# Performance work log

Measured on AMD Instinct MI355X. Metric: run time of the kernel, lower is better.

## Reference

```python
import jax, jax.numpy as jnp
import numpy as np

NUM_TABLES = 10
EMB_DIM = 3
VOCAB = 1_000_000
N_IDX = 4_000_000
N_BAGS = 100_000


def setup_inputs() -> dict:
    key = jax.random.key(0)
    k_idx, k_off, k_w = jax.random.split(key, 3)
    eb_input = jax.random.randint(k_idx, (N_IDX,), 0, VOCAB, dtype=jnp.int64)
    # EmbeddingBag offsets: sorted, first element must be 0, values in [0, N_IDX)
    eb_offset = jnp.sort(jax.random.randint(k_off, (N_BAGS,), 0, N_IDX, dtype=jnp.int64))
    eb_offset = eb_offset.at[0].set(0)
    # torch.nn.EmbeddingBag default init: N(0, 1)
    W = jax.random.normal(k_w, (NUM_TABLES, VOCAB, EMB_DIM), dtype=jnp.float32)
    return {"eb_input": eb_input, "eb_offset": eb_offset, "W": W}


def _bag_sums(eb_input, eb_offset, W):
    # segment id for each index position: bag b covers [offset[b], offset[b+1])
    n = eb_input.shape[0]
    seg = jnp.searchsorted(eb_offset, jnp.arange(n), side="right") - 1  # [N]
    gathered = W[:, eb_input, :]  # [T, N, D] irregular gather
    # sum-pool per bag for every table
    per_bag = jax.vmap(lambda g: jax.ops.segment_sum(g, seg, num_segments=eb_offset.shape[0]))(gathered)  # [T, B, D]
    return per_bag


def reference(eb_input, eb_offset, W):
    per_bag = _bag_sums(eb_input, eb_offset, W)  # [10, B, 3]
    outs = [per_bag[i] for i in range(NUM_TABLES)]
    outs[5] = jnp.sum(outs[5], axis=1, keepdims=True)  # [B, 1]
    outs[6] = jnp.sum(outs[6], axis=1, keepdims=True)  # [B, 1]
    cat = jnp.concatenate(outs, axis=1)  # [B, 26]
    return jnp.sum(cat, axis=0)  # [26]
```

## Files before the change

### kernel.cpp

```cpp
#include <hip/hip_runtime.h>

#define VOCAB 1000000
#define NUM_TABLES 10
#define OUT_SIZE 26
#define BUCKET_BITS 12
#define BPB 4096
#define NBUCKETS 245
#define CHUNK 4096
#define MAXSRC 1024
#define RBLOCKS_PER_TABLE 128
#define RTHREADS 256


__global__ void __launch_bounds__(256) scatter_kernel(
    const int* __restrict__ idx, int n,
    unsigned short* __restrict__ scat,
    unsigned int* __restrict__ gs32)
{
    __shared__ unsigned int lcount[256];
    __shared__ unsigned int sc[256];
    const int tid = threadIdx.x;
    lcount[tid] = 0u;
    __syncthreads();

    const int4* idx4 = (const int4*)idx;
    const int n4 = n >> 2;
    const int base4 = blockIdx.x * (CHUNK / 4);
    int4 q[4];
    bool val[4];
    unsigned rank[16];
    unsigned bkt[16];
#pragma unroll
    for (int j = 0; j < 4; ++j) {
        int i4 = base4 + j * 256 + tid;
        val[j] = (i4 < n4);
        if (val[j]) q[j] = idx4[i4];
    }
#pragma unroll
    for (int j = 0; j < 4; ++j) {
        if (val[j]) {
            unsigned v[4] = {(unsigned)q[j].x, (unsigned)q[j].y, (unsigned)q[j].z, (unsigned)q[j].w};
#pragma unroll
            for (int e = 0; e < 4; ++e) {
                bkt[j * 4 + e] = v[e] >> BUCKET_BITS;
                rank[j * 4 + e] = atomicAdd(&lcount[bkt[j * 4 + e]], 1u);
            }
        }
    }
    unsigned trank[3], tbkt[3];
    int tcnt = 0;
    if (blockIdx.x == gridDim.x - 1 && tid == 0) {
        for (int i = n4 * 4; i < n; ++i) {
            unsigned u = (unsigned)idx[i];
            tbkt[tcnt] = u >> BUCKET_BITS;
            trank[tcnt] = atomicAdd(&lcount[tbkt[tcnt]], 1u);
            ++tcnt;
        }
    }
    __syncthreads();
    unsigned cnt = (tid < NBUCKETS) ? lcount[tid] : 0u;
    sc[tid] = cnt;
    __syncthreads();
#pragma unroll
    for (int off = 1; off < 256; off <<= 1) {
        unsigned v = sc[tid];
        unsigned a = (tid >= off) ? sc[tid - off] : 0u;
        __syncthreads();
        sc[tid] = v + a;
        __syncthreads();
    }
    unsigned excl = sc[tid] - cnt;
    if (tid < NBUCKETS) gs32[tid * MAXSRC + blockIdx.x] = excl | (cnt << 16);
    lcount[tid] = excl;
    __syncthreads();
    unsigned short* myscat = scat + (size_t)blockIdx.x * CHUNK;
#pragma unroll
    for (int j = 0; j < 4; ++j) {
        if (val[j]) {
            unsigned v[4] = {(unsigned)q[j].x, (unsigned)q[j].y, (unsigned)q[j].z, (unsigned)q[j].w};
#pragma unroll
            for (int e = 0; e < 4; ++e) {
                unsigned k = j * 4 + e;
                myscat[lcount[bkt[k]] + rank[k]] = (unsigned short)(v[e] & (BPB - 1));
            }
        }
    }
    if (blockIdx.x == gridDim.x - 1 && tid == 0) {
        for (int i = 0; i < tcnt; ++i) {
            unsigned u = (unsigned)idx[n4 * 4 + i];
            myscat[lcount[tbkt[i]] + trank[i]] = (unsigned short)(u & (BPB - 1));
        }
    }
}

__device__ inline float wave_reduce(float v) {
#pragma unroll
    for (int o = 32; o > 0; o >>= 1) v += __shfl_down(v, o, 64);
    return v;
}

__global__ void __launch_bounds__(1024) fused_kernel(
    const unsigned short* __restrict__ scat,
    const unsigned int* __restrict__ gs32, int nsrc,
    const float* __restrict__ W,
    float* __restrict__ partials)
{
    __shared__ unsigned int h[BPB];
    const int b = blockIdx.x;
    const int tid = threadIdx.x;
    for (int i = tid; i < BPB; i += 1024) h[i] = 0u;
    __syncthreads();
    if (tid < nsrc) {
        unsigned g32 = gs32[b * MAXSRC + tid];
        unsigned s = g32 & 0xffffu, c = g32 >> 16;
        const unsigned short* p = scat + (size_t)tid * CHUNK + s;
        for (unsigned k = 0; k < c; ++k) atomicAdd(&h[p[k]], 1u);
    }
    __syncthreads();

    float acc[NUM_TABLES][3];
#pragma unroll
    for (int t = 0; t < NUM_TABLES; ++t) { acc[t][0] = 0.f; acc[t][1] = 0.f; acc[t][2] = 0.f; }

    const int ngroups = min(BPB / 4, (VOCAB - b * BPB) / 4);
    const int g = tid;
    if (g < ngroups) {
        uint4 c4 = ((const uint4*)h)[g];
        float c0 = (float)c4.x, c1 = (float)c4.y, c2 = (float)c4.z, c3 = (float)c4.w;
        size_t w4base = (size_t)b * 3072 + 3 * (size_t)g;
#pragma unroll
        for (int t = 0; t < NUM_TABLES; ++t) {
            const float4* W4 = ((const float4*)W) + (size_t)t * 750000 + w4base;
            float4 w0 = W4[0];
            float4 w1 = W4[1];
            float4 w2 = W4[2];
            acc[t][0] += c0 * w0.x + c1 * w0.w + c2 * w1.z + c3 * w2.y;
            acc[t][1] += c0 * w0.y + c1 * w1.x + c2 * w1.w + c3 * w2.z;
            acc[t][2] += c0 * w0.z + c1 * w1.y + c2 * w2.x + c3 * w2.w;
        }
    }
    __syncthreads();
    float* sf = (float*)h;
    const int wave = tid >> 6, lane = tid & 63;
#pragma unroll
    for (int t = 0; t < NUM_TABLES; ++t)
#pragma unroll
        for (int d = 0; d < 3; ++d) {
            float v = wave_reduce(acc[t][d]);
            if (lane == 0) sf[(t * 3 + d) * 16 + wave] = v;
        }
    __syncthreads();
    if (tid < 30) {
        float s = 0.f;
#pragma unroll
        for (int w = 0; w < 16; ++w) s += sf[tid * 16 + w];
        partials[b * 32 + tid] = s;
    }
}

__global__ void __launch_bounds__(256) final_kernel(const float* __restrict__ partials,
                                                    float* __restrict__ out) {
    __shared__ float red[256];
    __shared__ float tot[32];
    const int tid = threadIdx.x;
    const int v = tid & 31, c = tid >> 5;
    float s = 0.f;
    if (v < 30)
        for (int b = c; b < NBUCKETS; b += 8) s += partials[b * 32 + v];
    red[tid] = s;
    __syncthreads();
    if (tid < 32) {
        float t2 = 0.f;
#pragma unroll
        for (int cc = 0; cc < 8; ++cc) t2 += red[cc * 32 + tid];
        tot[tid] = t2;
    }
    __syncthreads();
    if (tid < OUT_SIZE) {
        float r;
        if (tid < 15) r = tot[tid];
        else if (tid == 15) r = tot[15] + tot[16] + tot[17];
        else if (tid == 16) r = tot[18] + tot[19] + tot[20];
        else r = tot[tid + 4];
        out[tid] = r;
    }
}


__global__ void zero_kernel_fb(unsigned int* __restrict__ hist, float* __restrict__ out) {
    int i = blockIdx.x * blockDim.x + threadIdx.x;
    int n4 = VOCAB / 4;
    if (i < n4) ((uint4*)hist)[i] = make_uint4(0u, 0u, 0u, 0u);
    if (i < OUT_SIZE) out[i] = 0.0f;
}

__global__ void hist_kernel_fb(const int* __restrict__ idx, unsigned int* __restrict__ hist, int n) {
    int i = blockIdx.x * blockDim.x + threadIdx.x;
    int i4 = i * 4;
    if (i4 + 3 < n) {
        int4 v = ((const int4*)idx)[i];
        atomicAdd(&hist[v.x], 1u);
        atomicAdd(&hist[v.y], 1u);
        atomicAdd(&hist[v.z], 1u);
        atomicAdd(&hist[v.w], 1u);
    } else {
        for (int j = i4; j < n; ++j) atomicAdd(&hist[idx[j]], 1u);
    }
}

__global__ void __launch_bounds__(RTHREADS) reduce_kernel_fb(const float* __restrict__ W,
                                                             const unsigned int* __restrict__ hist,
                                                             float* __restrict__ out) {
    const int t = blockIdx.x / RBLOCKS_PER_TABLE;
    const int b = blockIdx.x % RBLOCKS_PER_TABLE;
    const float4* __restrict__ W4 = (const float4*)(W + (size_t)t * VOCAB * 3);
    const uint4* __restrict__ h4 = (const uint4*)hist;
    const int ngroups = VOCAB / 4;
    float a0 = 0.f, a1 = 0.f, a2 = 0.f;
    const int stride = RBLOCKS_PER_TABLE * RTHREADS;
    for (int g = b * RTHREADS + (int)threadIdx.x; g < ngroups; g += stride) {
        uint4 c4 = h4[g];
        float4 w0 = W4[3 * g + 0];
        float4 w1 = W4[3 * g + 1];
        float4 w2 = W4[3 * g + 2];
        float c0 = (float)c4.x, c1 = (float)c4.y, c2 = (float)c4.z, c3 = (float)c4.w;
        a0 += c0 * w0.x + c1 * w0.w + c2 * w1.z + c3 * w2.y;
        a1 += c0 * w0.y + c1 * w1.x + c2 * w1.w + c3 * w2.z;
        a2 += c0 * w0.z + c1 * w1.y + c2 * w2.x + c3 * w2.w;
    }
    a0 = wave_reduce(a0);
    a1 = wave_reduce(a1);
    a2 = wave_reduce(a2);
    __shared__ float s[3][4];
    int wave = threadIdx.x >> 6;
    int lane = threadIdx.x & 63;
    if (lane == 0) { s[0][wave] = a0; s[1][wave] = a1; s[2][wave] = a2; }
    __syncthreads();
    if (threadIdx.x == 0) {
        float r0 = s[0][0] + s[0][1] + s[0][2] + s[0][3];
        float r1 = s[1][0] + s[1][1] + s[1][2] + s[1][3];
        float r2 = s[2][0] + s[2][1] + s[2][2] + s[2][3];
        if (t == 5) atomicAdd(&out[15], r0 + r1 + r2);
        else if (t == 6) atomicAdd(&out[16], r0 + r1 + r2);
        else {
            int base = (t < 5) ? t * 3 : 17 + (t - 7) * 3;
            atomicAdd(&out[base + 0], r0);
            atomicAdd(&out[base + 1], r1);
            atomicAdd(&out[base + 2], r2);
        }
    }
}


extern "C" void kernel_launch(void* const* d_in, const int* in_sizes, int n_in,
                              void* d_out, int out_size, void* d_ws, size_t ws_size,
                              hipStream_t stream) {
    const int* eb_input = (const int*)d_in[0];
    const float* W = (const float*)d_in[2];
    float* out = (float*)d_out;
    int n_idx = in_sizes[0];

    const int nsrc = (n_idx + CHUNK - 1) / CHUNK;
    const size_t scat_bytes = (size_t)MAXSRC * CHUNK * 2;
    const size_t gs_off = scat_bytes;
    const size_t gs_bytes = (size_t)NBUCKETS * MAXSRC * 4;
    const size_t part_off = gs_off + gs_bytes;
    const size_t need = part_off + (size_t)NBUCKETS * 32 * 4;

    if (nsrc <= MAXSRC && ws_size >= need) {
        unsigned short* scat = (unsigned short*)d_ws;
        unsigned int* gs32 = (unsigned int*)((char*)d_ws + gs_off);
        float* partials = (float*)((char*)d_ws + part_off);

        scatter_kernel<<<nsrc, 256, 0, stream>>>(eb_input, n_idx, scat, gs32);
        fused_kernel<<<NBUCKETS, 1024, 0, stream>>>(scat, gs32, nsrc, W, partials);
        final_kernel<<<1, 256, 0, stream>>>(partials, out);
    } else {
        unsigned int* hist = (unsigned int*)d_ws;
        int zblocks = (VOCAB / 4 + 255) / 256;
        zero_kernel_fb<<<zblocks, 256, 0, stream>>>(hist, out);
        int hthreads = (n_idx + 3) / 4;
        int hblocks = (hthreads + 255) / 256;
        hist_kernel_fb<<<hblocks, 256, 0, stream>>>(eb_input, hist, n_idx);
        reduce_kernel_fb<<<NUM_TABLES * RBLOCKS_PER_TABLE, RTHREADS, 0, stream>>>(W, hist, out);
    }
}
```

Baseline: 235.1 us.

## Split fused bucket kernel into histogram and wide reduce kernels, stage scatter in LDS

The per-bucket histogram-plus-weight kernel is split in two. A bucket histogram kernel writes a full global histogram, then a separate reduce kernel with many more blocks (10 tables × 256) streams W, writes per-block partials, and a new final kernel sums them. The goal is to spread the 120 MB W read across many more blocks than the 245 used before. The scatter kernel now stages its output in shared memory and writes it out with coalesced 16-byte stores, and the histogram loop is unrolled by four. The cost is an extra kernel launch plus a 4 MB histogram round trip through global memory.

```diff
diff --git a/kernel.cpp b/kernel.cpp
--- a/kernel.cpp
+++ b/kernel.cpp
@@ -8,7 +8,8 @@
 #define NBUCKETS 245
 #define CHUNK 4096
 #define MAXSRC 1024
-#define RBLOCKS_PER_TABLE 128
+#define RBLOCKS_PER_TABLE 256
+#define NRBLK (NUM_TABLES * RBLOCKS_PER_TABLE)
 #define RTHREADS 256
 
 
@@ -19,6 +20,7 @@
 {
     __shared__ unsigned int lcount[256];
     __shared__ unsigned int sc[256];
+    __shared__ unsigned short stage[CHUNK];
     const int tid = threadIdx.x;
     lcount[tid] = 0u;
     __syncthreads();
@@ -73,7 +75,6 @@
     if (tid < NBUCKETS) gs32[tid * MAXSRC + blockIdx.x] = excl | (cnt << 16);
     lcount[tid] = excl;
     __syncthreads();
-    unsigned short* myscat = scat + (size_t)blockIdx.x * CHUNK;
 #pragma unroll
     for (int j = 0; j < 4; ++j) {
         if (val[j]) {
@@ -81,29 +82,27 @@
 #pragma unroll
             for (int e = 0; e < 4; ++e) {
                 unsigned k = j * 4 + e;
-                myscat[lcount[bkt[k]] + rank[k]] = (unsigned short)(v[e] & (BPB - 1));
+                stage[lcount[bkt[k]] + rank[k]] = (unsigned short)(v[e] & (BPB - 1));
             }
         }
     }
     if (blockIdx.x == gridDim.x - 1 && tid == 0) {
         for (int i = 0; i < tcnt; ++i) {
             unsigned u = (unsigned)idx[n4 * 4 + i];
-            myscat[lcount[tbkt[i]] + trank[i]] = (unsigned short)(u & (BPB - 1));
-        }
-    }
-}
-
-__device__ inline float wave_reduce(float v) {
-#pragma unroll
-    for (int o = 32; o > 0; o >>= 1) v += __shfl_down(v, o, 64);
-    return v;
-}
-
-__global__ void __launch_bounds__(1024) fused_kernel(
+            stage[lcount[tbkt[i]] + trank[i]] = (unsigned short)(u & (BPB - 1));
+        }
+    }
+    __syncthreads();
+    uint4* dst = (uint4*)(scat + (size_t)blockIdx.x * CHUNK);
+    const uint4* src = (const uint4*)stage;
+#pragma unroll
+    for (int j = 0; j < 2; ++j) dst[j * 256 + tid] = src[j * 256 + tid];
+}
+
+__global__ void __launch_bounds__(1024) bucket_hist_kernel(
     const unsigned short* __restrict__ scat,
     const unsigned int* __restrict__ gs32, int nsrc,
-    const float* __restrict__ W,
-    float* __restrict__ partials)
+    unsigned int* __restrict__ hist)
 {
     __shared__ unsigned int h[BPB];
     const int b = blockIdx.x;
@@ -114,103 +113,32 @@
         unsigned g32 = gs32[b * MAXSRC + tid];
         unsigned s = g32 & 0xffffu, c = g32 >> 16;
         const unsigned short* p = scat + (size_t)tid * CHUNK + s;
-        for (unsigned k = 0; k < c; ++k) atomicAdd(&h[p[k]], 1u);
-    }
-    __syncthreads();
-
-    float acc[NUM_TABLES][3];
-#pragma unroll
-    for (int t = 0; t < NUM_TABLES; ++t) { acc[t][0] = 0.f; acc[t][1] = 0.f; acc[t][2] = 0.f; }
-
-    const int ngroups = min(BPB / 4, (VOCAB - b * BPB) / 4);
-    const int g = tid;
-    if (g < ngroups) {
-        uint4 c4 = ((const uint4*)h)[g];
-        float c0 = (float)c4.x, c1 = (float)c4.y, c2 = (float)c4.z, c3 = (float)c4.w;
-        size_t w4base = (size_t)b * 3072 + 3 * (size_t)g;
-#pragma unroll
-        for (int t = 0; t < NUM_TABLES; ++t) {
-            const float4* W4 = ((const float4*)W) + (size_t)t * 750000 + w4base;
-            float4 w0 = W4[0];
-            float4 w1 = W4[1];
-            float4 w2 = W4[2];
-            acc[t][0] += c0 * w0.x + c1 * w0.w + c2 * w1.z + c3 * w2.y;
-            acc[t][1] += c0 * w0.y + c1 * w1.x + c2 * w1.w + c3 * w2.z;
-            acc[t][2] += c0 * w0.z + c1 * w1.y + c2 * w2.x + c3 * w2.w;
-        }
-    }
-    __syncthreads();
-    float* sf = (float*)h;
-    const int wave = tid >> 6, lane = tid & 63;
-#pragma unroll
-    for (int t = 0; t < NUM_TABLES; ++t)
-#pragma unroll
-        for (int d = 0; d < 3; ++d) {
-            float v = wave_reduce(acc[t][d]);
-            if (lane == 0) sf[(t * 3 + d) * 16 + wave] = v;
-        }
-    __syncthreads();
-    if (tid < 30) {
-        float s = 0.f;
-#pragma unroll
-        for (int w = 0; w < 16; ++w) s += sf[tid * 16 + w];
-        partials[b * 32 + tid] = s;
-    }
-}
-
-__global__ void __launch_bounds__(256) final_kernel(const float* __restrict__ partials,
-                                                    float* __restrict__ out) {
-    __shared__ float red[256];
-    __shared__ float tot[32];
-    const int tid = threadIdx.x;
-    const int v = tid & 31, c = tid >> 5;
-    float s = 0.f;
-    if (v < 30)
-        for (int b = c; b < NBUCKETS; b += 8) s += partials[b * 32 + v];
-    red[tid] = s;
-    __syncthreads();
-    if (tid < 32) {
-        float t2 = 0.f;
-#pragma unroll
-        for (int cc = 0; cc < 8; ++cc) t2 += red[cc * 32 + tid];
-        tot[tid] = t2;
-    }
-    __syncthreads();
-    if (tid < OUT_SIZE) {
-        float r;
-        if (tid < 15) r = tot[tid];
-        else if (tid == 15) r = tot[15] + tot[16] + tot[17];
-        else if (tid == 16) r = tot[18] + tot[19] + tot[20];
-        else r = tot[tid + 4];
-        out[tid] = r;
-    }
-}
-
-
-__global__ void zero_kernel_fb(unsigned int* __restrict__ hist, float* __restrict__ out) {
-    int i = blockIdx.x * blockDim.x + threadIdx.x;
-    int n4 = VOCAB / 4;
-    if (i < n4) ((uint4*)hist)[i] = make_uint4(0u, 0u, 0u, 0u);
-    if (i < OUT_SIZE) out[i] = 0.0f;
-}
-
-__global__ void hist_kernel_fb(const int* __restrict__ idx, unsigned int* __restrict__ hist, int n) {
-    int i = blockIdx.x * blockDim.x + threadIdx.x;
-    int i4 = i * 4;
-    if (i4 + 3 < n) {
-        int4 v = ((const int4*)idx)[i];
-        atomicAdd(&hist[v.x], 1u);
-        atomicAdd(&hist[v.y], 1u);
-        atomicAdd(&hist[v.z], 1u);
-        atomicAdd(&hist[v.w], 1u);
-    } else {
-        for (int j = i4; j < n; ++j) atomicAdd(&hist[idx[j]], 1u);
-    }
-}
-
-__global__ void __launch_bounds__(RTHREADS) reduce_kernel_fb(const float* __restrict__ W,
-                                                             const unsigned int* __restrict__ hist,
-                                                             float* __restrict__ out) {
+        unsigned k = 0;
+        for (; k + 4 <= c; k += 4) {
+            unsigned short a0 = p[k], a1 = p[k + 1], a2 = p[k + 2], a3 = p[k + 3];
+            atomicAdd(&h[a0], 1u);
+            atomicAdd(&h[a1], 1u);
+            atomicAdd(&h[a2], 1u);
+            atomicAdd(&h[a3], 1u);
+        }
+        for (; k < c; ++k) atomicAdd(&h[p[k]], 1u);
+    }
+    __syncthreads();
+    int nb4 = min(BPB, VOCAB - b * BPB) >> 2;
+    uint4* dst = (uint4*)(hist + (size_t)b * BPB);
+    const uint4* src = (const uint4*)h;
+    if (tid < nb4) dst[tid] = src[tid];
+}
+
+__device__ inline float wave_reduce(float v) {
+#pragma unroll
+    for (int o = 32; o > 0; o >>= 1) v += __shfl_down(v, o, 64);
+    return v;
+}
+
+__global__ void __launch_bounds__(RTHREADS) reduce_kernel(const float* __restrict__ W,
+                                                          const unsigned int* __restrict__ hist,
+                                                          float* __restrict__ partials) {
     const int t = blockIdx.x / RBLOCKS_PER_TABLE;
     const int b = blockIdx.x % RBLOCKS_PER_TABLE;
     const float4* __restrict__ W4 = (const float4*)(W + (size_t)t * VOCAB * 3);
@@ -237,6 +165,90 @@
     if (lane == 0) { s[0][wave] = a0; s[1][wave] = a1; s[2][wave] = a2; }
     __syncthreads();
     if (threadIdx.x == 0) {
+        partials[0 * NRBLK + blockIdx.x] = s[0][0] + s[0][1] + s[0][2] + s[0][3];
+        partials[1 * NRBLK + blockIdx.x] = s[1][0] + s[1][1] + s[1][2] + s[1][3];
+        partials[2 * NRBLK + blockIdx.x] = s[2][0] + s[2][1] + s[2][2] + s[2][3];
+    }
+}
+
+__global__ void __launch_bounds__(1024) final_kernel(const float* __restrict__ partials,
+                                                     float* __restrict__ out) {
+    __shared__ float ts[32];
+    const int tid = threadIdx.x;
+    const int srs = tid >> 5;
+    const int j = tid & 31;
+    float v = 0.f;
+    if (srs < 30) {
+        const int t = srs / 3, d = srs % 3;
+        const float* p = partials + (size_t)d * NRBLK + t * RBLOCKS_PER_TABLE;
+#pragma unroll
+        for (int k = 0; k < RBLOCKS_PER_TABLE / 32; ++k) v += p[k * 32 + j];
+    }
+#pragma unroll
+    for (int off = 16; off > 0; off >>= 1) v += __shfl_down(v, off);
+    if (j == 0 && srs < 30) ts[srs] = v;
+    __syncthreads();
+    if (tid < OUT_SIZE) {
+        float r;
+        if (tid < 15) r = ts[tid];
+        else if (tid == 15) r = ts[15] + ts[16] + ts[17];
+        else if (tid == 16) r = ts[18] + ts[19] + ts[20];
+        else r = ts[tid + 4];
+        out[tid] = r;
+    }
+}
+
+
+__global__ void zero_kernel_fb(unsigned int* __restrict__ hist, float* __restrict__ out) {
+    int i = blockIdx.x * blockDim.x + threadIdx.x;
+    int n4 = VOCAB / 4;
+    if (i < n4) ((uint4*)hist)[i] = make_uint4(0u, 0u, 0u, 0u);
+    if (i < OUT_SIZE) out[i] = 0.0f;
+}
+
+__global__ void hist_kernel_fb(const int* __restrict__ idx, unsigned int* __restrict__ hist, int n) {
+    int i = blockIdx.x * blockDim.x + threadIdx.x;
+    int i4 = i * 4;
+    if (i4 + 3 < n) {
+        int4 v = ((const int4*)idx)[i];
+        atomicAdd(&hist[v.x], 1u);
+        atomicAdd(&hist[v.y], 1u);
+        atomicAdd(&hist[v.z], 1u);
+        atomicAdd(&hist[v.w], 1u);
+    } else {
+        for (int j = i4; j < n; ++j) atomicAdd(&hist[idx[j]], 1u);
+    }
+}
+
+__global__ void __launch_bounds__(RTHREADS) reduce_kernel_fb(const float* __restrict__ W,
+                                                             const unsigned int* __restrict__ hist,
+                                                             float* __restrict__ out) {
+    const int t = blockIdx.x / 64;
+    const int b = blockIdx.x % 64;
+    const float4* __restrict__ W4 = (const float4*)(W + (size_t)t * VOCAB * 3);
+    const uint4* __restrict__ h4 = (const uint4*)hist;
+    const int ngroups = VOCAB / 4;
+    float a0 = 0.f, a1 = 0.f, a2 = 0.f;
+    const int stride = 64 * RTHREADS;
+    for (int g = b * RTHREADS + (int)threadIdx.x; g < ngroups; g += stride) {
+        uint4 c4 = h4[g];
+        float4 w0 = W4[3 * g + 0];
+        float4 w1 = W4[3 * g + 1];
+        float4 w2 = W4[3 * g + 2];
+        float c0 = (float)c4.x, c1 = (float)c4.y, c2 = (float)c4.z, c3 = (float)c4.w;
+        a0 += c0 * w0.x + c1 * w0.w + c2 * w1.z + c3 * w2.y;
+        a1 += c0 * w0.y + c1 * w1.x + c2 * w1.w + c3 * w2.z;
+        a2 += c0 * w0.z + c1 * w1.y + c2 * w2.x + c3 * w2.w;
+    }
+    a0 = wave_reduce(a0);
+    a1 = wave_reduce(a1);
+    a2 = wave_reduce(a2);
+    __shared__ float s[3][4];
+    int wave = threadIdx.x >> 6;
+    int lane = threadIdx.x & 63;
+    if (lane == 0) { s[0][wave] = a0; s[1][wave] = a1; s[2][wave] = a2; }
+    __syncthreads();
+    if (threadIdx.x == 0) {
         float r0 = s[0][0] + s[0][1] + s[0][2] + s[0][3];
         float r1 = s[1][0] + s[1][1] + s[1][2] + s[1][3];
         float r2 = s[2][0] + s[2][1] + s[2][2] + s[2][3];
@@ -264,17 +276,21 @@
     const size_t scat_bytes = (size_t)MAXSRC * CHUNK * 2;
     const size_t gs_off = scat_bytes;
     const size_t gs_bytes = (size_t)NBUCKETS * MAXSRC * 4;
-    const size_t part_off = gs_off + gs_bytes;
-    const size_t need = part_off + (size_t)NBUCKETS * 32 * 4;
+    const size_t hist_off = gs_off + gs_bytes;
+    const size_t hist_bytes = (size_t)VOCAB * 4;
+    const size_t part_off = (hist_off + hist_bytes + 255) & ~(size_t)255;
+    const size_t need = part_off + (size_t)3 * NRBLK * 4;
 
     if (nsrc <= MAXSRC && ws_size >= need) {
         unsigned short* scat = (unsigned short*)d_ws;
         unsigned int* gs32 = (unsigned int*)((char*)d_ws + gs_off);
+        unsigned int* hist = (unsigned int*)((char*)d_ws + hist_off);
         float* partials = (float*)((char*)d_ws + part_off);
 
         scatter_kernel<<<nsrc, 256, 0, stream>>>(eb_input, n_idx, scat, gs32);
-        fused_kernel<<<NBUCKETS, 1024, 0, stream>>>(scat, gs32, nsrc, W, partials);
-        final_kernel<<<1, 256, 0, stream>>>(partials, out);
+        bucket_hist_kernel<<<NBUCKETS, 1024, 0, stream>>>(scat, gs32, nsrc, hist);
+        reduce_kernel<<<NRBLK, RTHREADS, 0, stream>>>(W, hist, partials);
+        final_kernel<<<1, 1024, 0, stream>>>(partials, out);
     } else {
         unsigned int* hist = (unsigned int*)d_ws;
         int zblocks = (VOCAB / 4 + 255) / 256;
@@ -282,6 +298,6 @@
         int hthreads = (n_idx + 3) / 4;
         int hblocks = (hthreads + 255) / 256;
         hist_kernel_fb<<<hblocks, 256, 0, stream>>>(eb_input, hist, n_idx);
-        reduce_kernel_fb<<<NUM_TABLES * RBLOCKS_PER_TABLE, RTHREADS, 0, stream>>>(W, hist, out);
-    }
-}
+        reduce_kernel_fb<<<NUM_TABLES * 64, RTHREADS, 0, stream>>>(W, hist, out);
+    }
+}
```

After: 209.2 us. 11.0% less time.
